# Kernel tuning notes

Hardware: AMD Instinct MI355X
Metric: run time of the kernel (lower is better)

The kernel has to match this reference:

```python
import jax, jax.numpy as jnp
import numpy as np

N_NODES = 100000
N_EDGES = 1600000
D_IN = 512
D_HID = 128
N_CLASSES = 100


def _gcn_norm(edge_index, n_nodes):
    # Add self loops and compute symmetric normalization D^{-1/2} (A+I) D^{-1/2}
    sl = jnp.arange(n_nodes, dtype=edge_index.dtype)
    src = jnp.concatenate([edge_index[0], sl])
    dst = jnp.concatenate([edge_index[1], sl])
    deg = jax.ops.segment_sum(jnp.ones_like(dst, dtype=jnp.float32), dst,
                              num_segments=n_nodes)
    dinv = jnp.where(deg > 0, jax.lax.rsqrt(deg), 0.0)
    norm = dinv[src] * dinv[dst]  # [E + N]
    return src, dst, norm


def _gcn_layer(x, W, b, src, dst, norm, n_nodes):
    h = x @ W                                  # [N, d_out] (transform first, like PyG GCNConv)
    msg = h[src] * norm[:, None]               # [E+N, d_out] gather + scale
    out = jax.ops.segment_sum(msg, dst, num_segments=n_nodes)  # scatter-add
    return out + b


def setup_inputs() -> dict:
    key = jax.random.key(0)
    ks = jax.random.split(key, 6)
    x = jax.random.normal(ks[0], (N_NODES, D_IN), dtype=jnp.float32)
    edge_index = jax.random.randint(ks[1], (2, N_EDGES), 0, N_NODES, dtype=jnp.int64)
    W1 = jax.random.normal(ks[2], (D_IN, D_HID), dtype=jnp.float32) * (1.0 / np.sqrt(D_IN))
    b1 = jnp.zeros((D_HID,), dtype=jnp.float32)
    W2 = jax.random.normal(ks[3], (D_HID, N_CLASSES), dtype=jnp.float32) * (1.0 / np.sqrt(D_HID))
    b2 = jnp.zeros((N_CLASSES,), dtype=jnp.float32)
    return {"x": x, "edge_index": edge_index, "W1": W1, "b1": b1, "W2": W2, "b2": b2}


def reference(x, edge_index, W1, b1, W2, b2):
    n_nodes = x.shape[0]
    src, dst, norm = _gcn_norm(edge_index, n_nodes)
    h = jax.nn.relu(_gcn_layer(x, W1, b1, src, dst, norm, n_nodes))
    logits = _gcn_layer(h, W2, b2, src, dst, norm, n_nodes)
    return jax.nn.log_softmax(logits, axis=-1)
```

## Files before the change

kernel.cpp:

```cpp
#include <hip/hip_runtime.h>
#include <math.h>

typedef __attribute__((ext_vector_type(8))) short short8;
typedef __attribute__((ext_vector_type(4))) float f32x4;
typedef _Float16 half8 __attribute__((ext_vector_type(8)));
typedef __fp16 fp16x2 __attribute__((ext_vector_type(2)));
typedef unsigned int uint;

__device__ inline uint f2bf(float f) {
    uint u = __float_as_uint(f);
    return (u + 0x7fffu + ((u >> 16) & 1u)) >> 16;
}
__device__ inline uint pack2(float lo, float hi) { return f2bf(lo) | (f2bf(hi) << 16); }
__device__ inline float bflo(uint u) { return __uint_as_float(u << 16); }
__device__ inline float bfhi(uint u) { return __uint_as_float(u & 0xffff0000u); }
__device__ inline uint cvtpk(float lo, float hi) {
    uint r;
    asm("v_cvt_pk_bf16_f32 %0, %1, %2" : "=v"(r) : "v"(lo), "v"(hi));
    return r;
}
__device__ inline uint pkh(float lo, float hi) {
    union { fp16x2 h; uint u; } c;
    c.h = __builtin_amdgcn_cvt_pkrtz(lo, hi);
    return c.u;
}
__device__ inline void gload16(const void* g, void* l) {
    __builtin_amdgcn_global_load_lds(
        (const __attribute__((address_space(1))) void*)g,
        (__attribute__((address_space(3))) void*)l, 16, 0, 0);
}

__global__ void k_degree(const int* __restrict__ dst, int E, int* __restrict__ cnt) {
    int i = blockIdx.x * 256 + threadIdx.x;
    if (i < E) atomicAdd(&cnt[dst[i]], 1);
}

__global__ void k_dinv(const int* __restrict__ cnt, float* __restrict__ dinv, int N) {
    int i = blockIdx.x * 256 + threadIdx.x;
    if (i < N) dinv[i] = rsqrtf((float)(cnt[i] + 1));
}

__global__ __launch_bounds__(512) void k_scan1(const int* __restrict__ cnt, int* __restrict__ rp,
                                               int* __restrict__ partials, int N) {
    __shared__ int s[512];
    int i = blockIdx.x * 512 + threadIdx.x;
    int v = (i < N) ? cnt[i] : 0;
    s[threadIdx.x] = v;
    __syncthreads();
    for (int d = 1; d < 512; d <<= 1) {
        int t = (threadIdx.x >= d) ? s[threadIdx.x - d] : 0;
        __syncthreads();
        s[threadIdx.x] += t;
        __syncthreads();
    }
    if (i < N) rp[i] = s[threadIdx.x] - v;
    if (threadIdx.x == 511) partials[blockIdx.x] = s[511];
}

__global__ void k_scan2(int* __restrict__ partials, int nb) {
    if (threadIdx.x == 0 && blockIdx.x == 0) {
        int acc = 0;
        for (int i = 0; i < nb; i++) { int v = partials[i]; partials[i] = acc; acc += v; }
    }
}

__global__ __launch_bounds__(512) void k_scan3(int* __restrict__ rp, const int* __restrict__ partials,
                                               int N, int E) {
    int i = blockIdx.x * 512 + threadIdx.x;
    if (i < N) rp[i] += partials[blockIdx.x];
    if (i == 0) rp[N] = E;
}

__global__ void k_fill(const int* __restrict__ src, const int* __restrict__ dst, int E,
                       const int* __restrict__ rp, int* __restrict__ cursor,
                       const float* __restrict__ dinv, float2* __restrict__ colw) {
    int i = blockIdx.x * 256 + threadIdx.x;
    if (i < E) {
        int d = dst[i];
        int s = src[i];
        int pos = rp[d] + atomicAdd(&cursor[d], 1);
        colw[pos] = make_float2(__int_as_float(s), dinv[s]);
    }
}

__global__ void k_w1prep(const float* __restrict__ W1, ushort* __restrict__ frag) {
    int tid = blockIdx.x * 256 + threadIdx.x;
    if (tid < 8192) {
        int ks = tid >> 9;
        int t = (tid >> 6) & 7;
        int l = tid & 63;
        int kbase = ks * 32 + (l >> 4) * 8;
        int c = t * 16 + (l & 15);
#pragma unroll
        for (int j = 0; j < 8; j++) {
            float v = W1[(size_t)(kbase + j) * 128 + c];
            union { _Float16 h; ushort u; } cv;
            cv.h = (_Float16)v;
            frag[(size_t)tid * 8 + j] = cv.u;
        }
    }
}

__global__ __launch_bounds__(256) void k_gemm1(const float* __restrict__ x,
                                               const uint4* __restrict__ w1f,
                                               uint* __restrict__ h1, int N) {
    __shared__ char lds[65536];
    int tid = threadIdx.x, wv = tid >> 6, l = tid & 63;
    int cl = l & 15, kg = l >> 4;
    int row0 = blockIdx.x * 32;
    int rhalf = wv & 1, chalf = wv >> 1;

    auto stageB = [&](int c) {
        char* bbase = lds + 32768 + (c & 1) * 16384;
        const char* bsrc = (const char*)w1f + (size_t)c * 16384;
#pragma unroll
        for (int i = 0; i < 4; i++) {
            int s = i * 256 + tid;
            gload16(bsrc + (size_t)s * 16, bbase + (size_t)(s - l) * 16);
        }
    };

    float4 xa[16];
#pragma unroll
    for (int p = 0; p < 16; p++) {
        int g4 = p * 256 + tid;
        int r = g4 >> 7;
        int rg = row0 + r; if (rg >= N) rg = N - 1;
        xa[p] = *(const float4*)(x + (size_t)rg * 512 + (size_t)(g4 & 127) * 4);
    }
    stageB(0);
#pragma unroll
    for (int p = 0; p < 16; p++) {
        int g4 = p * 256 + tid;
        int r = g4 >> 7;
        int f = g4 & 127;
        uint lo = pkh(xa[p].x, xa[p].y);
        uint hi = pkh(xa[p].z, xa[p].w);
        int gran = (f >> 1) ^ (r & 7);
        *(uint2*)(lds + (size_t)r * 1024 + gran * 16 + (f & 1) * 8) = make_uint2(lo, hi);
    }
    __syncthreads();

    f32x4 acc[4];
#pragma unroll
    for (int t = 0; t < 4; t++) acc[t] = (f32x4){0.f, 0.f, 0.f, 0.f};

    union U { uint4 u4; half8 h8; };
    int arow = rhalf * 16 + cl;

    for (int c = 0; c < 8; c++) {
        if (c < 7) stageB(c + 1);
        const char* bb = lds + 32768 + (c & 1) * 16384;
#pragma unroll
        for (int k2 = 0; k2 < 2; k2++) {
            int ks = c * 2 + k2;
            int slot = (ks * 4 + kg) ^ (arow & 7);
            U A;
            A.u4 = *(const uint4*)(lds + (size_t)arow * 1024 + slot * 16);
#pragma unroll
            for (int tt = 0; tt < 4; tt++) {
                U B;
                B.u4 = *(const uint4*)(bb + (size_t)(((k2 * 8 + chalf * 4 + tt) * 64 + l)) * 16);
                acc[tt] = __builtin_amdgcn_mfma_f32_16x16x32_f16(A.h8, B.h8, acc[tt], 0, 0, 0);
            }
        }
        __syncthreads();
    }

    uint* hsp = (uint*)lds + (size_t)wv * (16 * 33);
#pragma unroll
    for (int tt = 0; tt < 4; tt++)
#pragma unroll
        for (int r = 0; r < 4; r++) {
            float mine = acc[tt][r];
            float other = __shfl_xor(mine, 1, 64);
            if ((cl & 1) == 0)
                hsp[(kg * 4 + r) * 33 + tt * 8 + (cl >> 1)] = cvtpk(mine, other);
        }
#pragma unroll
    for (int p = 0; p < 8; p++) {
        int it = p * 2 + (l >> 5);
        int gr = row0 + rhalf * 16 + it;
        if (gr < N) h1[(size_t)gr * 64 + chalf * 32 + (l & 31)] = hsp[it * 33 + (l & 31)];
    }
}

template <bool RELU_BIAS>
__global__ __launch_bounds__(256) void k_agg(const uint* __restrict__ h, const float* __restrict__ dinv,
                                             const int* __restrict__ rp, const float2* __restrict__ colw,
                                             const float* __restrict__ bias, uint* __restrict__ outb, int N) {
    int wave = threadIdx.x >> 6, lane = threadIdx.x & 63;
    int v = blockIdx.x * 4 + wave;
    if (v >= N) return;
    float dv = dinv[v];
    float wself = dv * dv;
    uint us = h[(size_t)v * 64 + lane];
    float acc0 = bflo(us) * wself;
    float acc1 = bfhi(us) * wself;
    int e0 = rp[v], e1 = rp[v + 1];
    int i = e0;
    for (; i + 8 <= e1; i += 8) {
        float2 q[8];
        uint u[8];
#pragma unroll
        for (int j = 0; j < 8; j++) q[j] = colw[i + j];
#pragma unroll
        for (int j = 0; j < 8; j++) u[j] = h[(size_t)__float_as_int(q[j].x) * 64 + lane];
#pragma unroll
        for (int j = 0; j < 8; j++) {
            float w = q[j].y * dv;
            acc0 = fmaf(bflo(u[j]), w, acc0);
            acc1 = fmaf(bfhi(u[j]), w, acc1);
        }
    }
    if (i + 4 <= e1) {
        float2 q[4];
        uint u[4];
#pragma unroll
        for (int j = 0; j < 4; j++) q[j] = colw[i + j];
#pragma unroll
        for (int j = 0; j < 4; j++) u[j] = h[(size_t)__float_as_int(q[j].x) * 64 + lane];
#pragma unroll
        for (int j = 0; j < 4; j++) {
            float w = q[j].y * dv;
            acc0 = fmaf(bflo(u[j]), w, acc0);
            acc1 = fmaf(bfhi(u[j]), w, acc1);
        }
        i += 4;
    }
    for (; i < e1; i++) {
        float2 q = colw[i];
        uint u = h[(size_t)__float_as_int(q.x) * 64 + lane];
        float w = q.y * dv;
        acc0 = fmaf(bflo(u), w, acc0);
        acc1 = fmaf(bfhi(u), w, acc1);
    }
    if (RELU_BIAS) {
        float2 b = *(const float2*)&bias[2 * lane];
        acc0 = fmaxf(acc0 + b.x, 0.f);
        acc1 = fmaxf(acc1 + b.y, 0.f);
    }
    outb[(size_t)v * 64 + lane] = pack2(acc0, acc1);
}

__global__ void k_w2prep(const float* __restrict__ W2, const float* __restrict__ b2,
                         ushort* __restrict__ frag, float* __restrict__ b2pad) {
    int tid = blockIdx.x * 256 + threadIdx.x;
    if (tid < 1792) {
        int q = tid / 448;
        int t = (tid >> 6) % 7;
        int l = tid & 63;
        int kbase = q * 32 + (l >> 4) * 8;
        int c = t * 16 + (l & 15);
#pragma unroll
        for (int j = 0; j < 8; j++) {
            float v = (c < 100) ? W2[(kbase + j) * 100 + c] : 0.f;
            frag[(size_t)tid * 8 + j] = (ushort)f2bf(v);
        }
    } else if (tid < 1792 + 112) {
        int c = tid - 1792;
        b2pad[c] = (c < 100) ? b2[c] : -1e30f;
    }
}

__global__ __launch_bounds__(256) void k_out_mfma(const uint* __restrict__ g2u,
                                                  const uint4* __restrict__ w2fragG,
                                                  const float* __restrict__ b2pad,
                                                  float* __restrict__ out, int N) {
    __shared__ uint4 w2s[1792];
    __shared__ float b2s[112];
    int tid = threadIdx.x;
    for (int i = tid; i < 1792; i += 256) w2s[i] = w2fragG[i];
    if (tid < 112) b2s[tid] = b2pad[tid];
    __syncthreads();

    int w = tid >> 6, l = tid & 63;
    int v0 = blockIdx.x * 128 + w * 32;
    int cl = l & 15, gq = l >> 4;

    f32x4 acc[2][7];
#pragma unroll
    for (int m = 0; m < 2; m++)
#pragma unroll
        for (int t = 0; t < 7; t++) acc[m][t] = (f32x4){0.f, 0.f, 0.f, 0.f};

    union U { uint4 u4; short8 s8; };

#pragma unroll
    for (int q = 0; q < 4; q++) {
        short8 afr[2];
#pragma unroll
        for (int m = 0; m < 2; m++) {
            int rv = v0 + m * 16 + cl;
            if (rv >= N) rv = N - 1;
            U a;
            a.u4 = *(const uint4*)&g2u[(size_t)rv * 64 + q * 16 + gq * 4];
            afr[m] = a.s8;
        }
#pragma unroll
        for (int t = 0; t < 7; t++) {
            U b;
            b.u4 = w2s[(q * 7 + t) * 64 + l];
            acc[0][t] = __builtin_amdgcn_mfma_f32_16x16x32_bf16(afr[0], b.s8, acc[0][t], 0, 0, 0);
            acc[1][t] = __builtin_amdgcn_mfma_f32_16x16x32_bf16(afr[1], b.s8, acc[1][t], 0, 0, 0);
        }
    }

    float bsv[7];
#pragma unroll
    for (int t = 0; t < 7; t++) bsv[t] = b2s[t * 16 + cl];

#pragma unroll
    for (int m = 0; m < 2; m++) {
#pragma unroll
        for (int r = 0; r < 4; r++) {
            int row = v0 + m * 16 + gq * 4 + r;
            float lg[7];
#pragma unroll
            for (int t = 0; t < 7; t++) lg[t] = acc[m][t][r] + bsv[t];
            float mx = lg[0];
#pragma unroll
            for (int t = 1; t < 7; t++) mx = fmaxf(mx, lg[t]);
            mx = fmaxf(mx, __shfl_xor(mx, 1, 64));
            mx = fmaxf(mx, __shfl_xor(mx, 2, 64));
            mx = fmaxf(mx, __shfl_xor(mx, 4, 64));
            mx = fmaxf(mx, __shfl_xor(mx, 8, 64));
            float s = 0.f;
#pragma unroll
            for (int t = 0; t < 7; t++) s += __expf(lg[t] - mx);
            s += __shfl_xor(s, 1, 64);
            s += __shfl_xor(s, 2, 64);
            s += __shfl_xor(s, 4, 64);
            s += __shfl_xor(s, 8, 64);
            float lse = mx + __logf(s);
            if (row < N) {
#pragma unroll
                for (int t = 0; t < 7; t++) {
                    int c = t * 16 + cl;
                    if (c < 100) out[(size_t)row * 100 + c] = lg[t] - lse;
                }
            }
        }
    }
}

extern "C" void kernel_launch(void* const* d_in, const int* in_sizes, int n_in,
                              void* d_out, int out_size, void* d_ws, size_t ws_size,
                              hipStream_t stream) {
    const float* x  = (const float*)d_in[0];
    const int*   ei = (const int*)d_in[1];
    const float* W1 = (const float*)d_in[2];
    const float* b1 = (const float*)d_in[3];
    const float* W2 = (const float*)d_in[4];
    const float* b2 = (const float*)d_in[5];
    float* out = (float*)d_out;

    int N = in_sizes[0] / 512;
    int E = in_sizes[1] / 2;
    const int* srcI = ei;
    const int* dstI = ei + E;

    char* wsb = (char*)d_ws;
    size_t off = 0;
    auto alloc = [&](size_t bytes) {
        void* p = wsb + off;
        off = (off + bytes + 255) & ~(size_t)255;
        return p;
    };
    int*    cnt      = (int*)alloc((size_t)N * 4);
    int*    cursor   = (int*)alloc((size_t)N * 4);
    float*  dinv     = (float*)alloc((size_t)N * 4);
    int*    rp       = (int*)alloc((size_t)(N + 1) * 4);
    int*    partials = (int*)alloc(1024 * 4);
    ushort* w1f      = (ushort*)alloc(8192 * 8 * 2);
    ushort* w2frag   = (ushort*)alloc(1792 * 8 * 2);
    float*  b2pad    = (float*)alloc(112 * 4);
    float2* colw     = (float2*)alloc((size_t)E * 8);
    uint*   h1       = (uint*)alloc((size_t)N * 64 * 4);
    uint*   a1       = (uint*)alloc((size_t)N * 64 * 4);
    uint*   g2       = h1;

    hipMemsetAsync(cnt, 0, (size_t)N * 4, stream);
    hipMemsetAsync(cursor, 0, (size_t)N * 4, stream);

    k_degree<<<(E + 255) / 256, 256, 0, stream>>>(dstI, E, cnt);
    k_dinv<<<(N + 255) / 256, 256, 0, stream>>>(cnt, dinv, N);
    int nb = (N + 511) / 512;
    k_scan1<<<nb, 512, 0, stream>>>(cnt, rp, partials, N);
    k_scan2<<<1, 64, 0, stream>>>(partials, nb);
    k_scan3<<<nb, 512, 0, stream>>>(rp, partials, N, E);
    k_fill<<<(E + 255) / 256, 256, 0, stream>>>(srcI, dstI, E, rp, cursor, dinv, colw);
    k_w1prep<<<32, 256, 0, stream>>>(W1, w1f);
    k_w2prep<<<8, 256, 0, stream>>>(W2, b2, w2frag, b2pad);

    k_gemm1<<<(N + 31) / 32, 256, 0, stream>>>(x, (const uint4*)w1f, h1, N);
    k_agg<true><<<(N + 3) / 4, 256, 0, stream>>>(h1, dinv, rp, colw, b1, a1, N);
    k_agg<false><<<(N + 3) / 4, 256, 0, stream>>>(a1, dinv, rp, colw, nullptr, g2, N);
    k_out_mfma<<<(N + 127) / 128, 256, 0, stream>>>(g2, (const uint4*)w2frag, b2pad, out, N);
}
```

Before: 432.2 us.

## Stream x tiles through double-buffered LDS in gemm1 instead of preloading all

The first GEMM kernel no longer loads the whole 32x512 x tile into registers and LDS up front. It streams 64-column chunks through a double-buffered 8 KB LDS region, overlapping the global loads of x with the MFMA work of the previous chunk. LDS use drops from 64 KB to 40 KB, which may let more blocks share a CU, and register pressure from the 16 float4 preload goes away. The cost is a smaller prefetch depth per thread, so memory-level parallelism may be lower.

```diff
diff --git a/kernel.cpp b/kernel.cpp
--- a/kernel.cpp
+++ b/kernel.cpp
@@ -104,14 +104,18 @@
 __global__ __launch_bounds__(256) void k_gemm1(const float* __restrict__ x,
                                                const uint4* __restrict__ w1f,
                                                uint* __restrict__ h1, int N) {
-    __shared__ char lds[65536];
+    __shared__ __align__(16) char lds[40960];
     int tid = threadIdx.x, wv = tid >> 6, l = tid & 63;
     int cl = l & 15, kg = l >> 4;
     int row0 = blockIdx.x * 32;
     int rhalf = wv & 1, chalf = wv >> 1;
 
+    int xr = tid >> 3, xs = tid & 7;
+    int xrg = row0 + xr; if (xrg >= N) xrg = N - 1;
+    const float* xsrc = x + (size_t)xrg * 512 + xs * 8;
+
     auto stageB = [&](int c) {
-        char* bbase = lds + 32768 + (c & 1) * 16384;
+        char* bbase = lds + 8192 + (c & 1) * 16384;
         const char* bsrc = (const char*)w1f + (size_t)c * 16384;
 #pragma unroll
         for (int i = 0; i < 4; i++) {
@@ -120,26 +124,21 @@
         }
     };
 
-    float4 xa[16];
-#pragma unroll
-    for (int p = 0; p < 16; p++) {
-        int g4 = p * 256 + tid;
-        int r = g4 >> 7;
-        int rg = row0 + r; if (rg >= N) rg = N - 1;
-        xa[p] = *(const float4*)(x + (size_t)rg * 512 + (size_t)(g4 & 127) * 4);
-    }
-    stageB(0);
-#pragma unroll
-    for (int p = 0; p < 16; p++) {
-        int g4 = p * 256 + tid;
-        int r = g4 >> 7;
-        int f = g4 & 127;
-        uint lo = pkh(xa[p].x, xa[p].y);
-        uint hi = pkh(xa[p].z, xa[p].w);
-        int gran = (f >> 1) ^ (r & 7);
-        *(uint2*)(lds + (size_t)r * 1024 + gran * 16 + (f & 1) * 8) = make_uint2(lo, hi);
-    }
-    __syncthreads();
+    float4 f0, f1;
+    auto loadx = [&](int c) {
+        const float* p = xsrc + c * 64;
+        f0 = *(const float4*)p;
+        f1 = *(const float4*)(p + 4);
+    };
+    auto writex = [&](int c) {
+        char* xb = lds + (c & 1) * 4096;
+        uint4 v;
+        v.x = pkh(f0.x, f0.y);
+        v.y = pkh(f0.z, f0.w);
+        v.z = pkh(f1.x, f1.y);
+        v.w = pkh(f1.z, f1.w);
+        *(uint4*)(xb + xr * 128 + ((xs ^ (xr & 7)) * 16)) = v;
+    };
 
     f32x4 acc[4];
 #pragma unroll
@@ -148,15 +147,19 @@
     union U { uint4 u4; half8 h8; };
     int arow = rhalf * 16 + cl;
 
+    loadx(0);
+    stageB(0);
+    writex(0);
+    __syncthreads();
+
     for (int c = 0; c < 8; c++) {
-        if (c < 7) stageB(c + 1);
-        const char* bb = lds + 32768 + (c & 1) * 16384;
+        if (c < 7) { loadx(c + 1); stageB(c + 1); }
+        const char* xb = lds + (c & 1) * 4096;
+        const char* bb = lds + 8192 + (c & 1) * 16384;
 #pragma unroll
         for (int k2 = 0; k2 < 2; k2++) {
-            int ks = c * 2 + k2;
-            int slot = (ks * 4 + kg) ^ (arow & 7);
             U A;
-            A.u4 = *(const uint4*)(lds + (size_t)arow * 1024 + slot * 16);
+            A.u4 = *(const uint4*)(xb + arow * 128 + (((k2 * 4 + kg) ^ (arow & 7)) * 16));
 #pragma unroll
             for (int tt = 0; tt < 4; tt++) {
                 U B;
@@ -164,6 +167,7 @@
                 acc[tt] = __builtin_amdgcn_mfma_f32_16x16x32_f16(A.h8, B.h8, acc[tt], 0, 0, 0);
             }
         }
+        if (c < 7) writex(c + 1);
         __syncthreads();
     }
 
```

After: 402.2 us. 1.07x faster.
